# Optimization experiments

Hardware: AMD Instinct MI355X
Metric: run time of the kernel (lower is better)

## Reference

```python
import jax, jax.numpy as jnp
import numpy as np

EPS = 1e-5

def _bn(z, g, b, m, v):
    # eval-mode BatchNorm2d over channel axis 1 of [N,C,T,V]
    inv = g / jnp.sqrt(v + EPS)
    return z * inv[None, :, None, None] + (b - m * inv)[None, :, None, None]

def setup_inputs() -> dict:
    key = jax.random.key(0)
    ks = jax.random.split(key, 16)
    N, C, T, V, K, Cout, KT = 64, 64, 300, 25, 3, 64, 9
    x = jax.random.normal(ks[0], (N, C, T, V), dtype=jnp.float32)
    A = jax.random.normal(ks[1], (N, K, V, V), dtype=jnp.float32) * 0.2
    conv_w = jax.random.normal(ks[2], (K * Cout, C), dtype=jnp.float32) * (1.0 / np.sqrt(C))
    conv_b = jax.random.normal(ks[3], (K * Cout,), dtype=jnp.float32) * 0.01
    bn1_g = jax.random.uniform(ks[4], (Cout,), dtype=jnp.float32, minval=0.5, maxval=1.5)
    bn1_b = jax.random.normal(ks[5], (Cout,), dtype=jnp.float32) * 0.1
    bn1_m = jax.random.normal(ks[6], (Cout,), dtype=jnp.float32) * 0.1
    bn1_v = jax.random.uniform(ks[7], (Cout,), dtype=jnp.float32, minval=0.5, maxval=1.5)
    tconv_w = jax.random.normal(ks[8], (Cout, Cout, KT, 1), dtype=jnp.float32) * (1.0 / np.sqrt(Cout * KT))
    tconv_b = jax.random.normal(ks[9], (Cout,), dtype=jnp.float32) * 0.01
    bn2_g = jax.random.uniform(ks[10], (Cout,), dtype=jnp.float32, minval=0.5, maxval=1.5)
    bn2_b = jax.random.normal(ks[11], (Cout,), dtype=jnp.float32) * 0.1
    bn2_m = jax.random.normal(ks[12], (Cout,), dtype=jnp.float32) * 0.1
    bn2_v = jax.random.uniform(ks[13], (Cout,), dtype=jnp.float32, minval=0.5, maxval=1.5)
    return {"x": x, "A": A, "conv_w": conv_w, "conv_b": conv_b,
            "bn1_g": bn1_g, "bn1_b": bn1_b, "bn1_m": bn1_m, "bn1_v": bn1_v,
            "tconv_w": tconv_w, "tconv_b": tconv_b,
            "bn2_g": bn2_g, "bn2_b": bn2_b, "bn2_m": bn2_m, "bn2_v": bn2_v}

def reference(x, A, conv_w, conv_b, bn1_g, bn1_b, bn1_m, bn1_v,
              tconv_w, tconv_b, bn2_g, bn2_b, bn2_m, bn2_v):
    N, C, T, V = x.shape
    K = A.shape[1]
    Cout = conv_w.shape[0] // K
    # GCN: 1x1 conv producing K*Cout channels, then spatial aggregation via A
    y = jnp.einsum('nctv,oc->notv', x, conv_w) + conv_b[None, :, None, None]
    y = y.reshape(N, K, Cout, T, V)
    z = jnp.einsum('nkctv,nkvw->nctw', y, A)  # [N, Cout, T, V]
    # TCN: BN -> ReLU -> temporal conv (KTx1, pad (KT-1)//2) -> BN -> (dropout=0)
    h = jax.nn.relu(_bn(z, bn1_g, bn1_b, bn1_m, bn1_v))
    KT = tconv_w.shape[2]
    pad = (KT - 1) // 2
    h = jax.lax.conv_general_dilated(h, tconv_w, window_strides=(1, 1),
                                     padding=((pad, pad), (0, 0)),
                                     dimension_numbers=('NCHW', 'OIHW', 'NCHW'))
    h = h + tconv_b[None, :, None, None]
    h = _bn(h, bn2_g, bn2_b, bn2_m, bn2_v)
    # residual is identity (in_channels == out_channels, stride 1)
    out = jax.nn.relu(h + x)
    return (out, A)
```

## Files before the change

kernel.cpp:

```cpp
#include <hip/hip_runtime.h>

typedef float f32x4 __attribute__((ext_vector_type(4)));
typedef short bf16x8 __attribute__((ext_vector_type(8)));
typedef unsigned short u16;

namespace {

constexpr int Nn = 64, Tt = 300, Vv = 25;
constexpr float EPSf = 1e-5f;

__device__ __forceinline__ u16 f2bu(float f) {
  union { float f; unsigned int i; } c; c.f = f;
  unsigned int r = c.i + 0x7fffu + ((c.i >> 16) & 1u);
  return (u16)(r >> 16);
}

__global__ __launch_bounds__(256) void prep(
    const float* __restrict__ A, const float* __restrict__ Wc, const float* __restrict__ bc,
    const float* __restrict__ g1, const float* __restrict__ b1,
    const float* __restrict__ m1, const float* __restrict__ v1,
    const float* __restrict__ tcw, const float* __restrict__ tb,
    const float* __restrict__ g2, const float* __restrict__ b2,
    const float* __restrict__ m2, const float* __restrict__ v2,
    u16* __restrict__ atk, u16* __restrict__ wt, u16* __restrict__ w2t,
    float* __restrict__ invadd, float* __restrict__ bias2d,
    float* __restrict__ outA)
{
  const int b = blockIdx.x, tid = threadIdx.x;
  if (b < 64) {
    __shared__ float Al[1875];
    __shared__ float SAl[75];
    const float* An = A + b * 1875;
    for (int e = tid; e < 1875; e += 256) Al[e] = An[e];
    __syncthreads();
    if (tid < 75) {
      int k = tid / 25, w = tid % 25;
      float s = 0.f;
      for (int v = 0; v < 25; ++v) s += Al[k * 625 + v * 25 + w];
      SAl[tid] = s;
    }
    for (int e = tid; e < 1875; e += 256) outA[b * 1875 + e] = Al[e];
    __syncthreads();
    for (int e = tid; e < 3072; e += 256) {
      int k = e >> 10, r = e & 1023, w = r >> 5, v = r & 31;
      float val = (v < 25 && w < 25) ? Al[k * 625 + v * 25 + w] : 0.f;
      atk[b * 3072 + e] = f2bu(val);
    }
    for (int e = tid; e < 1600; e += 256) {
      int c = e / 25, w = e % 25;
      bias2d[b * 1600 + e] = bc[c] * SAl[w] + bc[64 + c] * SAl[25 + w] + bc[128 + c] * SAl[50 + w];
    }
  } else if (b == 64) {
    for (int e = tid; e < 12288; e += 256) {
      int c = e / 192, r = e - c * 192, k = r >> 6, ci = r & 63;
      wt[e] = f2bu(Wc[(k * 64 + c) * 64 + ci]);
    }
    if (tid < 64) {
      int c = tid;
      float i1 = g1[c] * rsqrtf(v1[c] + EPSf);
      float a1 = b1[c] - m1[c] * i1;
      float i2 = g2[c] * rsqrtf(v2[c] + EPSf);
      float a2 = b2[c] - m2[c] * i2 + tb[c] * i2;
      invadd[c] = i1; invadd[64 + c] = a1; invadd[128 + c] = i2; invadd[192 + c] = a2;
    }
  } else {
    const int kt = b - 65;
    for (int i = tid; i < 4096; i += 256) {
      int co = i >> 6, ci = i & 63;
      w2t[kt * 4096 + i] = f2bu(tcw[(co * 64 + ci) * 9 + kt]);
    }
  }
}

__global__ __launch_bounds__(512, 4) void k1_gcn(
    const float* __restrict__ x, const u16* __restrict__ atk, const u16* __restrict__ wt,
    const float* __restrict__ invadd, const float* __restrict__ bias2d,
    u16* __restrict__ zT)
{
  __shared__ __align__(16) u16 xaT[160 * 192];
  __shared__ float bias_l[1600];

  const int tid = threadIdx.x;
  const int tt = blockIdx.x, n = blockIdx.y;
  const int t0 = tt * 6;
  const int w = tid >> 6, l = tid & 63, lq = l & 15, g = l >> 4;
  const int ct = w & 3, h = w >> 2;
  const int co0 = ct * 16;

  for (int e = tid; e < 1600; e += 512) bias_l[e] = bias2d[n * 1600 + e];
  for (int e = tid; e < 10 * 192; e += 512) xaT[150 * 192 + e] = 0;

  bf16x8 Bf[3][2];
  #pragma unroll
  for (int k = 0; k < 3; ++k)
    #pragma unroll
    for (int nt = 0; nt < 2; ++nt)
      Bf[k][nt] = *(const bf16x8*)(atk + ((size_t)(n * 3 + k) * 32 + nt * 16 + lq) * 32 + g * 8);

  bf16x8 wf1[6];
  #pragma unroll
  for (int kc = 0; kc < 6; ++kc)
    wf1[kc] = *(const bf16x8*)(wt + (co0 + lq) * 192 + kc * 32 + g * 8);

  f32x4 xc0, xc1;
  {
    const int mt = w;
    const int tl = mt >> 2, ci0 = (mt & 3) << 4;
    const float* xr = x + ((size_t)(n * 64 + ci0 + lq) * Tt + t0 + tl) * Vv;
    __builtin_memcpy(&xc0, xr + g * 8, 16);
    __builtin_memcpy(&xc1, xr + g * 8 + 4, 16);
  }
  #pragma unroll 1
  for (int i = 0; i < 3; ++i) {
    f32x4 xn0, xn1;
    if (i < 2) {
      const int mtn = w + 8 * (i + 1);
      const int tln = mtn >> 2, ci0n = (mtn & 3) << 4;
      const float* xrn = x + ((size_t)(n * 64 + ci0n + lq) * Tt + t0 + tln) * Vv;
      __builtin_memcpy(&xn0, xrn + g * 8, 16);
      __builtin_memcpy(&xn1, xrn + g * 8 + 4, 16);
    }
    const int mt = w + 8 * i;
    const int tl = mt >> 2, ci0 = (mt & 3) << 4;
    bf16x8 a;
    if (g < 3) {
      a[0] = (short)f2bu(xc0[0]); a[1] = (short)f2bu(xc0[1]);
      a[2] = (short)f2bu(xc0[2]); a[3] = (short)f2bu(xc0[3]);
      a[4] = (short)f2bu(xc1[0]); a[5] = (short)f2bu(xc1[1]);
      a[6] = (short)f2bu(xc1[2]); a[7] = (short)f2bu(xc1[3]);
    } else {
      a[0] = (short)f2bu(xc0[0]);
      a[1] = 0; a[2] = 0; a[3] = 0; a[4] = 0; a[5] = 0; a[6] = 0; a[7] = 0;
    }
    #pragma unroll
    for (int k = 0; k < 3; ++k)
      #pragma unroll
      for (int nt = 0; nt < 2; ++nt) {
        f32x4 acc = {0.f, 0.f, 0.f, 0.f};
        acc = __builtin_amdgcn_mfma_f32_16x16x32_bf16(a, Bf[k][nt], acc, 0, 0, 0);
        const int wcol = nt * 16 + lq;
        if (wcol < 25) {
          const int twl = tl * 25 + wcol;
          ushort4 s;
          s.x = f2bu(acc[0]); s.y = f2bu(acc[1]); s.z = f2bu(acc[2]); s.w = f2bu(acc[3]);
          const int byte = twl * 384 + ((k * 128 + ci0 * 2 + g * 8) ^ ((twl & 7) << 4));
          *(ushort4*)((char*)xaT + byte) = s;
        }
      }
    xc0 = xn0; xc1 = xn1;
  }
  __syncthreads();

  f32x4 acc[5];
  #pragma unroll
  for (int j = 0; j < 5; ++j) acc[j] = (f32x4){0.f, 0.f, 0.f, 0.f};

  #pragma unroll
  for (int kc = 0; kc < 6; ++kc) {
    #pragma unroll
    for (int j = 0; j < 5; ++j) {
      const int row = (h * 5 + j) * 16 + lq;
      const int byte = row * 384 + ((kc * 64 + g * 16) ^ ((row & 7) << 4));
      const bf16x8 Bv = *(const bf16x8*)((const char*)xaT + byte);
      acc[j] = __builtin_amdgcn_mfma_f32_16x16x32_bf16(wf1[kc], Bv, acc[j], 0, 0, 0);
    }
  }

  const int c0 = co0 + g * 4;
  const f32x4 iv = *(const f32x4*)(invadd + c0);
  const f32x4 av = *(const f32x4*)(invadd + 64 + c0);
  #pragma unroll
  for (int j = 0; j < 5; ++j) {
    const int twl = (h * 5 + j) * 16 + lq;
    if (twl < 150) {
      const int wcol = twl % 25;
      const int tvg = tt * 150 + twl;
      ushort4 s;
      float z0 = (acc[j][0] + bias_l[(c0 + 0) * 25 + wcol]) * iv[0] + av[0];
      float z1 = (acc[j][1] + bias_l[(c0 + 1) * 25 + wcol]) * iv[1] + av[1];
      float z2 = (acc[j][2] + bias_l[(c0 + 2) * 25 + wcol]) * iv[2] + av[2];
      float z3 = (acc[j][3] + bias_l[(c0 + 3) * 25 + wcol]) * iv[3] + av[3];
      s.x = f2bu(fmaxf(z0, 0.f)); s.y = f2bu(fmaxf(z1, 0.f));
      s.z = f2bu(fmaxf(z2, 0.f)); s.w = f2bu(fmaxf(z3, 0.f));
      *(ushort4*)(zT + ((size_t)n * 7500 + tvg) * 64 + c0) = s;
    }
  }
}

__global__ __launch_bounds__(512, 4) void k2_tcn(
    const u16* __restrict__ zT, const u16* __restrict__ w2t,
    const float* __restrict__ invadd, const float* __restrict__ x,
    float* __restrict__ out)
{
  __shared__ __align__(16) u16 win[512 * 64];

  const int tid = threadIdx.x;
  const int tt = blockIdx.x, n = blockIdx.y;
  const int t0 = tt * 12;
  const int w = tid >> 6, l = tid & 63, lq = l & 15, g = l >> 4;
  const int ct = w & 3, h = w >> 2;
  const int co0 = ct * 16;
  const int tvbase = t0 * 25 - 100;

  #pragma unroll
  for (int it = 0; it < 8; ++it) {
    const int f = tid + it * 512;
    const int lrow = f >> 3, c16 = f & 7;
    const int tv = tvbase + lrow;
    bf16x8 val = {0, 0, 0, 0, 0, 0, 0, 0};
    if (tv >= 0 && tv < 7500)
      val = *(const bf16x8*)(zT + ((size_t)n * 7500 + tv) * 64 + c16 * 8);
    const int byte = lrow * 128 + ((c16 * 16) ^ ((lrow & 7) << 4));
    *(bf16x8*)((char*)win + byte) = val;
  }
  __syncthreads();

  const int nj = h ? 9 : 10;
  const u16* wbase = w2t + (co0 + lq) * 64 + g * 8;
  const float i2 = invadd[128 + co0 + lq];
  const float a2 = invadd[192 + co0 + lq];

  #pragma unroll 1
  for (int jh = 0; jh < 2; ++jh) {
    const int jlim = jh ? (nj - 5) : 5;
    const int mt0 = h * 10 + jh * 5;

    f32x4 acc[5];
    #pragma unroll
    for (int j = 0; j < 5; ++j) acc[j] = (f32x4){0.f, 0.f, 0.f, 0.f};

    #pragma unroll 1
    for (int kc = 0; kc < 2; ++kc) {
      bf16x8 wf[9];
      #pragma unroll
      for (int kt = 0; kt < 9; ++kt)
        wf[kt] = *(const bf16x8*)(wbase + (size_t)kt * 4096 + kc * 32);
      #pragma unroll
      for (int kt = 0; kt < 9; ++kt) {
        #pragma unroll
        for (int j = 0; j < 5; ++j) {
          if (j < jlim) {
            const int lrow = (mt0 + j) * 16 + lq + kt * 25;
            const int byte = lrow * 128 + ((kc * 64 + g * 16) ^ ((lrow & 7) << 4));
            const bf16x8 Av = *(const bf16x8*)((const char*)win + byte);
            acc[j] = __builtin_amdgcn_mfma_f32_16x16x32_bf16(Av, wf[kt], acc[j], 0, 0, 0);
          }
        }
      }
    }

    #pragma unroll
    for (int j = 0; j < 5; ++j) {
      if (j < jlim) {
        const int tvl0 = (mt0 + j) * 16 + g * 4;
        if (tvl0 < 300) {
          const size_t base = (size_t)(n * 64 + co0 + lq) * 7500 + t0 * 25 + tvl0;
          const f32x4 xv = *(const f32x4*)(x + base);
          f32x4 o;
          #pragma unroll
          for (int r = 0; r < 4; ++r)
            o[r] = fmaxf(acc[j][r] * i2 + a2 + xv[r], 0.f);
          *(f32x4*)(out + base) = o;
        }
      }
    }
  }
}

}

extern "C" void kernel_launch(void* const* d_in, const int* in_sizes, int n_in,
                              void* d_out, int out_size, void* d_ws, size_t ws_size,
                              hipStream_t stream)
{
  const float* x  = (const float*)d_in[0];
  const float* A  = (const float*)d_in[1];
  const float* Wc = (const float*)d_in[2];
  const float* bc = (const float*)d_in[3];
  const float* g1 = (const float*)d_in[4];
  const float* b1 = (const float*)d_in[5];
  const float* m1 = (const float*)d_in[6];
  const float* v1 = (const float*)d_in[7];
  const float* tw = (const float*)d_in[8];
  const float* tb = (const float*)d_in[9];
  const float* g2 = (const float*)d_in[10];
  const float* b2 = (const float*)d_in[11];
  const float* m2 = (const float*)d_in[12];
  const float* v2 = (const float*)d_in[13];
  float* out = (float*)d_out;

  char* ws = (char*)d_ws;
  u16*   zT     = (u16*)(ws);
  u16*   atk    = (u16*)(ws + 61440000);
  u16*   wt     = (u16*)(ws + 61833216);
  u16*   w2t    = (u16*)(ws + 61857792);
  float* invadd = (float*)(ws + 61931520);
  float* bias2d = (float*)(ws + 61932544);

  prep<<<dim3(74), dim3(256), 0, stream>>>(A, Wc, bc, g1, b1, m1, v1, tw, tb,
                                           g2, b2, m2, v2, atk, wt, w2t, invadd, bias2d,
                                           out + 30720000);
  k1_gcn<<<dim3(50, 64), dim3(512), 0, stream>>>(x, atk, wt, invadd, bias2d, zT);
  k2_tcn<<<dim3(25, 64), dim3(512), 0, stream>>>(zT, w2t, invadd, x, out);
}
```

Measured before the change: 195.0 us.

## Retile TCN kernel so each wave covers two output-channel tiles per LDS A-fragment

Changes the per-wave work split in the temporal-conv kernel. Each wave now computes two 16-channel output tiles over five row tiles, so every LDS A-fragment read feeds two MFMAs instead of one, halving LDS traffic per MFMA. Weights are loaded in chunks of three taps to limit register use. The cost is ten accumulator vectors per wave instead of five, which raises register pressure under the launch bound of 4 blocks, and the last wave group handles only four row tiles, leaving some imbalance.

```diff
diff --git a/kernel.cpp b/kernel.cpp
--- a/kernel.cpp
+++ b/kernel.cpp
@@ -198,8 +198,8 @@
   const int tt = blockIdx.x, n = blockIdx.y;
   const int t0 = tt * 12;
   const int w = tid >> 6, l = tid & 63, lq = l & 15, g = l >> 4;
-  const int ct = w & 3, h = w >> 2;
-  const int co0 = ct * 16;
+  const int ctp = w & 1, q = w >> 1;
+  const int co0 = ctp * 32;
   const int tvbase = t0 * 25 - 100;
 
   #pragma unroll
@@ -215,51 +215,59 @@
   }
   __syncthreads();
 
-  const int nj = h ? 9 : 10;
-  const u16* wbase = w2t + (co0 + lq) * 64 + g * 8;
-  const float i2 = invadd[128 + co0 + lq];
-  const float a2 = invadd[192 + co0 + lq];
+  const int jlim = (q < 3) ? 5 : 4;
+  const int mt0 = q * 5;
+  const u16* wb0 = w2t + (co0 + lq) * 64 + g * 8;
+  const u16* wb1 = w2t + (co0 + 16 + lq) * 64 + g * 8;
+
+  f32x4 acc[5][2];
+  #pragma unroll
+  for (int j = 0; j < 5; ++j)
+    #pragma unroll
+    for (int p = 0; p < 2; ++p) acc[j][p] = (f32x4){0.f, 0.f, 0.f, 0.f};
 
   #pragma unroll 1
-  for (int jh = 0; jh < 2; ++jh) {
-    const int jlim = jh ? (nj - 5) : 5;
-    const int mt0 = h * 10 + jh * 5;
-
-    f32x4 acc[5];
-    #pragma unroll
-    for (int j = 0; j < 5; ++j) acc[j] = (f32x4){0.f, 0.f, 0.f, 0.f};
-
+  for (int kc = 0; kc < 2; ++kc) {
     #pragma unroll 1
-    for (int kc = 0; kc < 2; ++kc) {
-      bf16x8 wf[9];
+    for (int ch = 0; ch < 3; ++ch) {
+      bf16x8 wf[3][2];
       #pragma unroll
-      for (int kt = 0; kt < 9; ++kt)
-        wf[kt] = *(const bf16x8*)(wbase + (size_t)kt * 4096 + kc * 32);
+      for (int k3 = 0; k3 < 3; ++k3) {
+        wf[k3][0] = *(const bf16x8*)(wb0 + (size_t)(ch * 3 + k3) * 4096 + kc * 32);
+        wf[k3][1] = *(const bf16x8*)(wb1 + (size_t)(ch * 3 + k3) * 4096 + kc * 32);
+      }
       #pragma unroll
-      for (int kt = 0; kt < 9; ++kt) {
+      for (int k3 = 0; k3 < 3; ++k3) {
         #pragma unroll
         for (int j = 0; j < 5; ++j) {
           if (j < jlim) {
-            const int lrow = (mt0 + j) * 16 + lq + kt * 25;
+            const int lrow = (mt0 + j) * 16 + lq + (ch * 3 + k3) * 25;
             const int byte = lrow * 128 + ((kc * 64 + g * 16) ^ ((lrow & 7) << 4));
             const bf16x8 Av = *(const bf16x8*)((const char*)win + byte);
-            acc[j] = __builtin_amdgcn_mfma_f32_16x16x32_bf16(Av, wf[kt], acc[j], 0, 0, 0);
+            acc[j][0] = __builtin_amdgcn_mfma_f32_16x16x32_bf16(Av, wf[k3][0], acc[j][0], 0, 0, 0);
+            acc[j][1] = __builtin_amdgcn_mfma_f32_16x16x32_bf16(Av, wf[k3][1], acc[j][1], 0, 0, 0);
           }
         }
       }
     }
-
+  }
+
+  #pragma unroll
+  for (int p = 0; p < 2; ++p) {
+    const int co = co0 + p * 16 + lq;
+    const float i2 = invadd[128 + co];
+    const float a2 = invadd[192 + co];
     #pragma unroll
     for (int j = 0; j < 5; ++j) {
       if (j < jlim) {
         const int tvl0 = (mt0 + j) * 16 + g * 4;
         if (tvl0 < 300) {
-          const size_t base = (size_t)(n * 64 + co0 + lq) * 7500 + t0 * 25 + tvl0;
+          const size_t base = (size_t)(n * 64 + co) * 7500 + t0 * 25 + tvl0;
           const f32x4 xv = *(const f32x4*)(x + base);
           f32x4 o;
           #pragma unroll
           for (int r = 0; r < 4; ++r)
-            o[r] = fmaxf(acc[j][r] * i2 + a2 + xv[r], 0.f);
+            o[r] = fmaxf(acc[j][p][r] * i2 + a2 + xv[r], 0.f);
           *(f32x4*)(out + base) = o;
         }
       }
```

Measured after the change: 216.1 us. 10.8% more time.
